# Kernel optimization log

Measured on AMD Instinct MI355X. Metric: run time of the kernel, lower is better.

## Reference

```python
import jax, jax.numpy as jnp
import numpy as np

EPS = 1e-06

def setup_inputs() -> dict:
    key = jax.random.key(0)
    k1, k2, k3, k4, k5 = jax.random.split(key, 5)
    B, T, D, Dv = 4, 2048, 128, 128
    q = jax.random.normal(k1, (B, T, D), dtype=jnp.float32)
    k = jax.random.normal(k2, (B, T, D), dtype=jnp.float32)
    v = jax.random.normal(k3, (B, T, Dv), dtype=jnp.float32)
    # phi = nn.Linear(dim, dim) followed by ELU; torch Linear default init ~ U(-1/sqrt(D), 1/sqrt(D))
    lim = 1.0 / np.sqrt(D)
    W_phi = jax.random.uniform(k4, (D, D), minval=-lim, maxval=lim, dtype=jnp.float32)
    b_phi = jax.random.uniform(k5, (D,), minval=-lim, maxval=lim, dtype=jnp.float32)
    return {"q": q, "k": k, "v": v, "W_phi": W_phi, "b_phi": b_phi}

def reference(q, k, v, W_phi, b_phi):
    # feature map: phi(x) = ELU(x @ W^T + b) + 1  (positive features)
    def phi(x):
        return jax.nn.elu(jnp.einsum('btd,ed->bte', x, W_phi) + b_phi) + 1.0

    Q = phi(q)                      # [B,T,D]
    K = phi(k)                      # [B,T,D]
    # causal recurrent state (zero initial state since h=None):
    # z_t = sum_{tau<=t} K_tau                 -> [B,T,D]
    # s_t = sum_{tau<=t} K_tau (outer) v_tau   -> [B,T,D,Dv]
    z = jnp.cumsum(K, axis=1)
    s = jnp.cumsum(K[..., :, None] * v[..., None, :], axis=1)
    den = jnp.einsum('btd,btd->bt', Q, z) + EPS          # [B,T]
    out = jnp.einsum('btd,btde->bte', Q, s) / den[..., None]  # [B,T,Dv]
    return out
```

## Files before the change

kernel.cpp:

```cpp
#include <hip/hip_runtime.h>
#include <hip/hip_bf16.h>

#define BB 4
#define TT 2048
#define DD 128
#define CHK 64
#define NCHK 32
#define NCHKS (BB*NCHK)

typedef __attribute__((ext_vector_type(8))) short  bf16x8;
typedef __attribute__((ext_vector_type(4))) float  f32x4;

#define MFMA(a,b,c) __builtin_amdgcn_mfma_f32_16x16x32_bf16(a, b, c, 0, 0, 0)

__device__ __forceinline__ short f2b(float f) {
    union { float f; unsigned u; } x; x.f = f;
    unsigned r = x.u + 0x7fffu + ((x.u >> 16) & 1u);
    return (short)(r >> 16);
}
__device__ __forceinline__ float b2f(short s) {
    union { unsigned u; float f; } x; x.u = ((unsigned)(unsigned short)s) << 16;
    return x.f;
}
__device__ __forceinline__ bf16x8 cvt8(const float* p) {
    float4 a = *(const float4*)p, b = *(const float4*)(p + 4);
    bf16x8 r;
    r[0]=f2b(a.x); r[1]=f2b(a.y); r[2]=f2b(a.z); r[3]=f2b(a.w);
    r[4]=f2b(b.x); r[5]=f2b(b.y); r[6]=f2b(b.z); r[7]=f2b(b.w);
    return r;
}

__global__ __launch_bounds__(256, 2) void k1_chunk(const float* __restrict__ q,
                                                   const float* __restrict__ kin,
                                                   const float* __restrict__ vin,
                                                   const float* __restrict__ W,
                                                   const float* __restrict__ bias,
                                                   short* __restrict__ Ss_g,
                                                   float* __restrict__ zc_g,
                                                   short* __restrict__ vT_g,
                                                   short* __restrict__ Qf_g,
                                                   short* __restrict__ Kf_g) {
    int c = blockIdx.x >> 1, dh = blockIdx.x & 1;
    int d0 = 64 * dh;
    const float* qc = q   + (size_t)c * CHK * DD;
    const float* kc = kin + (size_t)c * CHK * DD;
    const float* vc = vin + (size_t)c * CHK * DD;

    __shared__ __align__(16) short Wl [64][DD + 8];
    __shared__ __align__(16) short KfT[64][CHK + 8];
    __shared__ __align__(16) short vT [DD][CHK + 8];
    __shared__ __align__(16) short stage[2][CHK][CHK + 8];

    int tid = threadIdx.x, lane = tid & 63, w = tid >> 6;
    int l15 = lane & 15, l4 = lane >> 4;
    const f32x4 z4 = {0.f, 0.f, 0.f, 0.f};

    bf16x8 afk[4], afq[4];
    {
        int row = 16 * w + l15;
        #pragma unroll
        for (int kk = 0; kk < 4; ++kk) {
            afk[kk] = cvt8(kc + row * DD + kk * 32 + l4 * 8);
            afq[kk] = cvt8(qc + row * DD + kk * 32 + l4 * 8);
        }
    }
    #pragma unroll
    for (int it = 0; it < 8; ++it) {
        int i = tid + it * 256;
        int row = i >> 5, c4 = (i & 31) * 4;
        float4 v = *(const float4*)(W + (size_t)(d0 + row) * DD + c4);
        unsigned lo = (unsigned short)f2b(v.x) | ((unsigned)(unsigned short)f2b(v.y) << 16);
        unsigned hi = (unsigned short)f2b(v.z) | ((unsigned)(unsigned short)f2b(v.w) << 16);
        uint2 p; p.x = lo; p.y = hi;
        *(uint2*)&Wl[row][c4] = p;
    }
    #pragma unroll
    for (int it = 0; it < 8; ++it) {
        int i = tid + it * 256;
        int t = i >> 5, e4 = (i & 31) * 4;
        float4 vv = *(const float4*)(vc + t * DD + e4);
        vT[e4 + 0][t] = f2b(vv.x); vT[e4 + 1][t] = f2b(vv.y);
        vT[e4 + 2][t] = f2b(vv.z); vT[e4 + 3][t] = f2b(vv.w);
    }
    __syncthreads();

    #pragma unroll
    for (int n = 0; n < 4; ++n) {
        int dl = 16 * n + l15;
        f32x4 dk = z4, dq = z4;
        #pragma unroll
        for (int kk = 0; kk < 4; ++kk) {
            bf16x8 bw = *(const bf16x8*)&Wl[dl][kk * 32 + l4 * 8];
            dk = MFMA(afk[kk], bw, dk);
            dq = MFMA(afq[kk], bw, dq);
        }
        float bv = bias[d0 + dl];
        #pragma unroll
        for (int j = 0; j < 4; ++j) {
            int t = 16 * w + l4 * 4 + j;
            float zk = dk[j] + bv;
            short rk = f2b((zk > 0.f) ? (zk + 1.f) : __expf(zk));
            KfT[dl][t] = rk;
            stage[0][t][dl] = rk;
            float zq = dq[j] + bv;
            stage[1][t][dl] = f2b((zq > 0.f) ? (zq + 1.f) : __expf(zq));
        }
    }
    __syncthreads();

    {
        short* dk_ = Kf_g + (size_t)c * CHK * DD + d0;
        short* dq_ = Qf_g + (size_t)c * CHK * DD + d0;
        #pragma unroll
        for (int it = 0; it < 2; ++it) {
            int i = tid + it * 256;
            int t = i >> 3, u = (i & 7) * 8;
            *(bf16x8*)(dk_ + t * DD + u) = *(const bf16x8*)&stage[0][t][u];
            *(bf16x8*)(dq_ + t * DD + u) = *(const bf16x8*)&stage[1][t][u];
        }
    }
    if (tid < 64) {
        float s = 0.f;
        #pragma unroll
        for (int t8 = 0; t8 < CHK / 8; ++t8) {
            bf16x8 kv = *(const bf16x8*)&KfT[tid][t8 * 8];
            #pragma unroll
            for (int j = 0; j < 8; ++j) s += b2f(kv[j]);
        }
        zc_g[(size_t)c * DD + d0 + tid] = s;
    }
    if (dh == 0) {
        #pragma unroll
        for (int it = 0; it < 4; ++it) {
            int i = tid + it * 256;
            int e = i >> 3, t0 = (i & 7) * 8;
            *(bf16x8*)(vT_g + (size_t)c * DD * CHK + e * CHK + t0) =
                *(const bf16x8*)&vT[e][t0];
        }
    }

    f32x4 sacc[8];
    #pragma unroll
    for (int n = 0; n < 8; ++n) sacc[n] = z4;
    #pragma unroll
    for (int kk = 0; kk < 2; ++kk) {
        bf16x8 afr = *(const bf16x8*)&KfT[16 * w + l15][kk * 32 + l4 * 8];
        #pragma unroll
        for (int n = 0; n < 8; ++n) {
            bf16x8 bfr = *(const bf16x8*)&vT[16 * n + l15][kk * 32 + l4 * 8];
            sacc[n] = MFMA(afr, bfr, sacc[n]);
        }
    }
    __syncthreads();

    short (*st)[CHK + 8] = (short(*)[CHK + 8])&stage[0][0][0];
    #pragma unroll
    for (int n = 0; n < 8; ++n) {
        int e = 16 * n + l15;
        #pragma unroll
        for (int j = 0; j < 4; ++j)
            st[e][16 * w + l4 * 4 + j] = f2b(sacc[n][j]);
    }
    __syncthreads();

    short* dst = Ss_g + (size_t)c * DD * DD + d0;
    #pragma unroll
    for (int it = 0; it < 4; ++it) {
        int i = tid + it * 256;
        int e = i >> 3, u = (i & 7) * 8;
        *(bf16x8*)(dst + e * DD + u) = *(const bf16x8*)&st[e][u];
    }
}

__global__ __launch_bounds__(128) void k2_scan(const short* __restrict__ Ss_g,
                                               const float* __restrict__ zc_g,
                                               short* __restrict__ Sp_g,
                                               float* __restrict__ zp_g) {
    int e = blockIdx.x & 127, b = blockIdx.x >> 7;
    int d = threadIdx.x;
    size_t base = ((size_t)(b * NCHK) * DD + e) * DD + d;
    const size_t stride = (size_t)DD * DD;

    float vals[NCHK];
    #pragma unroll
    for (int c2 = 0; c2 < NCHK; ++c2) vals[c2] = b2f(Ss_g[base + c2 * stride]);
    float run = 0.f;
    #pragma unroll
    for (int c2 = 0; c2 < NCHK; ++c2) {
        Sp_g[base + c2 * stride] = f2b(run);
        run += vals[c2];
    }
    if (e == 0) {
        float vz[NCHK];
        #pragma unroll
        for (int c2 = 0; c2 < NCHK; ++c2) vz[c2] = zc_g[(size_t)(b * NCHK + c2) * DD + d];
        float rz = 0.f;
        #pragma unroll
        for (int c2 = 0; c2 < NCHK; ++c2) {
            zp_g[(size_t)(b * NCHK + c2) * DD + d] = rz;
            rz += vz[c2];
        }
    }
}

__global__ __launch_bounds__(256) void k3_out(const short* __restrict__ Qf_g,
                                              const short* __restrict__ Kf_g,
                                              const short* __restrict__ Sp_g,
                                              const float* __restrict__ zp_g,
                                              const short* __restrict__ vT_g,
                                              float* __restrict__ out) {
    int c = blockIdx.x >> 1, h = blockIdx.x & 1;

    __shared__ __align__(16) short Qf[CHK][DD + 8];
    __shared__ __align__(16) short Kf[CHK][DD + 8];
    __shared__ __align__(16) short Ps[CHK][CHK + 8];
    __shared__ float den[CHK];

    int tid = threadIdx.x, lane = tid & 63, w = tid >> 6;
    int l15 = lane & 15, l4 = lane >> 4;
    const f32x4 z4 = {0.f, 0.f, 0.f, 0.f};

    const float* zp = zp_g + (size_t)c * DD;
    bf16x8 bz[4];
    #pragma unroll
    for (int kk = 0; kk < 4; ++kk) {
        bf16x8 zf = cvt8(zp + kk * 32 + l4 * 8);
        bf16x8 zero = {0,0,0,0,0,0,0,0};
        bz[kk] = (l15 == 0) ? zf : zero;
    }

    {
        const short* srcq = Qf_g + (size_t)c * CHK * DD;
        const short* srck = Kf_g + (size_t)c * CHK * DD;
        #pragma unroll
        for (int it = 0; it < 4; ++it) {
            int i = tid + it * 256;
            int t = i >> 4, u = (i & 15) * 8;
            *(bf16x8*)&Qf[t][u] = *(const bf16x8*)(srcq + t * DD + u);
            *(bf16x8*)&Kf[t][u] = *(const bf16x8*)(srck + t * DD + u);
        }
    }
    __syncthreads();

    bf16x8 aq[4];
    #pragma unroll
    for (int kk = 0; kk < 4; ++kk)
        aq[kk] = *(const bf16x8*)&Qf[16 * w + l15][kk * 32 + l4 * 8];

    f32x4 p4 = z4;
    #pragma unroll
    for (int kk = 0; kk < 4; ++kk) p4 = MFMA(aq[kk], bz[kk], p4);

    float rs[4] = {0.f, 0.f, 0.f, 0.f};
    #pragma unroll
    for (int n2 = 0; n2 < 4; ++n2) {
        f32x4 p = z4;
        #pragma unroll
        for (int kk = 0; kk < 4; ++kk) {
            bf16x8 bk = *(const bf16x8*)&Kf[16 * n2 + l15][kk * 32 + l4 * 8];
            p = MFMA(aq[kk], bk, p);
        }
        int t2 = 16 * n2 + l15;
        #pragma unroll
        for (int j = 0; j < 4; ++j) {
            int t = 16 * w + l4 * 4 + j;
            float pm = (t2 <= t) ? p[j] : 0.f;
            Ps[t][t2] = f2b(pm);
            rs[j] += pm;
        }
    }
    #pragma unroll
    for (int off = 1; off < 16; off <<= 1) {
        #pragma unroll
        for (int j = 0; j < 4; ++j) rs[j] += __shfl_xor(rs[j], off);
    }
    if (l15 == 0) {
        #pragma unroll
        for (int j = 0; j < 4; ++j)
            den[16 * w + l4 * 4 + j] = rs[j] + p4[j] + 1e-6f;
    }

    bf16x8 ap[2];
    #pragma unroll
    for (int kk = 0; kk < 2; ++kk)
        ap[kk] = *(const bf16x8*)&Ps[16 * w + l15][kk * 32 + l4 * 8];

    const short* Sp  = Sp_g + (size_t)c * DD * DD;
    const short* vTg = vT_g + (size_t)c * DD * CHK;
    f32x4 oacc[4];
    #pragma unroll
    for (int n = 0; n < 4; ++n) oacc[n] = z4;
    #pragma unroll
    for (int n = 0; n < 4; ++n) {
        int e = 64 * h + 16 * n + l15;
        #pragma unroll
        for (int kk = 0; kk < 4; ++kk) {
            bf16x8 bs = *(const bf16x8*)(Sp + e * DD + kk * 32 + l4 * 8);
            oacc[n] = MFMA(aq[kk], bs, oacc[n]);
        }
        #pragma unroll
        for (int kk = 0; kk < 2; ++kk) {
            bf16x8 bv = *(const bf16x8*)(vTg + e * CHK + kk * 32 + l4 * 8);
            oacc[n] = MFMA(ap[kk], bv, oacc[n]);
        }
    }

    float* oc = out + (size_t)c * CHK * DD;
    float invs[4];
    #pragma unroll
    for (int j = 0; j < 4; ++j) invs[j] = 1.0f / den[16 * w + l4 * 4 + j];
    #pragma unroll
    for (int n = 0; n < 4; ++n) {
        int e = 64 * h + 16 * n + l15;
        #pragma unroll
        for (int j = 0; j < 4; ++j) {
            int t = 16 * w + l4 * 4 + j;
            oc[t * DD + e] = oacc[n][j] * invs[j];
        }
    }
}

extern "C" void kernel_launch(void* const* d_in, const int* in_sizes, int n_in,
                              void* d_out, int out_size, void* d_ws, size_t ws_size,
                              hipStream_t stream) {
    const float* q  = (const float*)d_in[0];
    const float* k  = (const float*)d_in[1];
    const float* v  = (const float*)d_in[2];
    const float* W  = (const float*)d_in[3];
    const float* bi = (const float*)d_in[4];
    float* out = (float*)d_out;

    float* zc_g = (float*)d_ws;
    float* zp_g = zc_g + (size_t)NCHKS * DD;
    short* Ss_g = (short*)(zp_g + (size_t)NCHKS * DD);
    short* Sp_g = Ss_g + (size_t)NCHKS * DD * DD;
    short* vT_g = Sp_g + (size_t)NCHKS * DD * DD;
    short* Qf_g = vT_g + (size_t)NCHKS * DD * CHK;
    short* Kf_g = Qf_g + (size_t)NCHKS * CHK * DD;

    k1_chunk<<<2 * NCHKS, 256, 0, stream>>>(q, k, v, W, bi, Ss_g, zc_g, vT_g, Qf_g, Kf_g);
    k2_scan<<<512, 128, 0, stream>>>(Ss_g, zc_g, Sp_g, zp_g);
    k3_out<<<2 * NCHKS, 256, 0, stream>>>(Qf_g, Kf_g, Sp_g, zp_g, vT_g, out);
}
```

Before: 27.02 us.

## Merge split-D chunk blocks into one 1024-thread block per chunk

The first kernel now runs one 1024-thread block per chunk instead of two 256-thread blocks that each handle half of the feature dimension. This stops duplicating the q/k/v loads and the v transpose across the two half-blocks, and q/k are staged through LDS so all 16 waves share them. In exchange, there are only 128 blocks on the GPU, each with a much larger LDS footprint, which lowers occupancy and parallelism. The block also adds an extra barrier.

```diff
diff --git a/kernel.cpp b/kernel.cpp
--- a/kernel.cpp
+++ b/kernel.cpp
@@ -30,53 +30,51 @@
     return r;
 }
 
-__global__ __launch_bounds__(256, 2) void k1_chunk(const float* __restrict__ q,
-                                                   const float* __restrict__ kin,
-                                                   const float* __restrict__ vin,
-                                                   const float* __restrict__ W,
-                                                   const float* __restrict__ bias,
-                                                   short* __restrict__ Ss_g,
-                                                   float* __restrict__ zc_g,
-                                                   short* __restrict__ vT_g,
-                                                   short* __restrict__ Qf_g,
-                                                   short* __restrict__ Kf_g) {
-    int c = blockIdx.x >> 1, dh = blockIdx.x & 1;
-    int d0 = 64 * dh;
+__global__ __launch_bounds__(1024) void k1_chunk(const float* __restrict__ q,
+                                                 const float* __restrict__ kin,
+                                                 const float* __restrict__ vin,
+                                                 const float* __restrict__ W,
+                                                 const float* __restrict__ bias,
+                                                 short* __restrict__ Ss_g,
+                                                 float* __restrict__ zc_g,
+                                                 short* __restrict__ vT_g,
+                                                 short* __restrict__ Qf_g,
+                                                 short* __restrict__ Kf_g) {
+    int c = blockIdx.x;
     const float* qc = q   + (size_t)c * CHK * DD;
     const float* kc = kin + (size_t)c * CHK * DD;
     const float* vc = vin + (size_t)c * CHK * DD;
 
-    __shared__ __align__(16) short Wl [64][DD + 8];
-    __shared__ __align__(16) short KfT[64][CHK + 8];
+    __shared__ __align__(16) short Wl [DD][DD + 8];
+    __shared__ __align__(16) short qs [CHK][DD + 8];
+    __shared__ __align__(16) short ks [CHK][DD + 8];
+    __shared__ __align__(16) short KfT[DD][CHK + 8];
     __shared__ __align__(16) short vT [DD][CHK + 8];
-    __shared__ __align__(16) short stage[2][CHK][CHK + 8];
+    __shared__ __align__(16) short st [DD][DD + 8];
 
     int tid = threadIdx.x, lane = tid & 63, w = tid >> 6;
     int l15 = lane & 15, l4 = lane >> 4;
+    int tq = w & 3, eh = w >> 2;
     const f32x4 z4 = {0.f, 0.f, 0.f, 0.f};
 
-    bf16x8 afk[4], afq[4];
-    {
-        int row = 16 * w + l15;
-        #pragma unroll
-        for (int kk = 0; kk < 4; ++kk) {
-            afk[kk] = cvt8(kc + row * DD + kk * 32 + l4 * 8);
-            afq[kk] = cvt8(qc + row * DD + kk * 32 + l4 * 8);
-        }
-    }
-    #pragma unroll
-    for (int it = 0; it < 8; ++it) {
-        int i = tid + it * 256;
+    #pragma unroll
+    for (int it = 0; it < 4; ++it) {
+        int i = tid + it * 1024;
         int row = i >> 5, c4 = (i & 31) * 4;
-        float4 v = *(const float4*)(W + (size_t)(d0 + row) * DD + c4);
+        float4 v = *(const float4*)(W + (size_t)row * DD + c4);
         unsigned lo = (unsigned short)f2b(v.x) | ((unsigned)(unsigned short)f2b(v.y) << 16);
         unsigned hi = (unsigned short)f2b(v.z) | ((unsigned)(unsigned short)f2b(v.w) << 16);
         uint2 p; p.x = lo; p.y = hi;
         *(uint2*)&Wl[row][c4] = p;
     }
-    #pragma unroll
-    for (int it = 0; it < 8; ++it) {
-        int i = tid + it * 256;
+    {
+        int row = tid >> 4, col8 = (tid & 15) * 8;
+        *(bf16x8*)&qs[row][col8] = cvt8(qc + row * DD + col8);
+        *(bf16x8*)&ks[row][col8] = cvt8(kc + row * DD + col8);
+    }
+    #pragma unroll
+    for (int it = 0; it < 2; ++it) {
+        int i = tid + it * 1024;
         int t = i >> 5, e4 = (i & 31) * 4;
         float4 vv = *(const float4*)(vc + t * DD + e4);
         vT[e4 + 0][t] = f2b(vv.x); vT[e4 + 1][t] = f2b(vv.y);
@@ -84,42 +82,47 @@
     }
     __syncthreads();
 
-    #pragma unroll
-    for (int n = 0; n < 4; ++n) {
-        int dl = 16 * n + l15;
-        f32x4 dk = z4, dq = z4;
+    bf16x8 afq[4], afk[4];
+    {
+        int row = 16 * tq + l15;
         #pragma unroll
         for (int kk = 0; kk < 4; ++kk) {
-            bf16x8 bw = *(const bf16x8*)&Wl[dl][kk * 32 + l4 * 8];
+            afq[kk] = *(const bf16x8*)&qs[row][kk * 32 + l4 * 8];
+            afk[kk] = *(const bf16x8*)&ks[row][kk * 32 + l4 * 8];
+        }
+    }
+    __syncthreads();
+
+    #pragma unroll
+    for (int n = 0; n < 2; ++n) {
+        int e = 32 * eh + 16 * n + l15;
+        f32x4 dq = z4, dk = z4;
+        #pragma unroll
+        for (int kk = 0; kk < 4; ++kk) {
+            bf16x8 bw = *(const bf16x8*)&Wl[e][kk * 32 + l4 * 8];
+            dq = MFMA(afq[kk], bw, dq);
             dk = MFMA(afk[kk], bw, dk);
-            dq = MFMA(afq[kk], bw, dq);
-        }
-        float bv = bias[d0 + dl];
+        }
+        float bv = bias[e];
         #pragma unroll
         for (int j = 0; j < 4; ++j) {
-            int t = 16 * w + l4 * 4 + j;
+            int t = 16 * tq + l4 * 4 + j;
+            float zq = dq[j] + bv;
+            qs[t][e] = f2b((zq > 0.f) ? (zq + 1.f) : __expf(zq));
             float zk = dk[j] + bv;
             short rk = f2b((zk > 0.f) ? (zk + 1.f) : __expf(zk));
-            KfT[dl][t] = rk;
-            stage[0][t][dl] = rk;
-            float zq = dq[j] + bv;
-            stage[1][t][dl] = f2b((zq > 0.f) ? (zq + 1.f) : __expf(zq));
-        }
-    }
-    __syncthreads();
-
-    {
-        short* dk_ = Kf_g + (size_t)c * CHK * DD + d0;
-        short* dq_ = Qf_g + (size_t)c * CHK * DD + d0;
-        #pragma unroll
-        for (int it = 0; it < 2; ++it) {
-            int i = tid + it * 256;
-            int t = i >> 3, u = (i & 7) * 8;
-            *(bf16x8*)(dk_ + t * DD + u) = *(const bf16x8*)&stage[0][t][u];
-            *(bf16x8*)(dq_ + t * DD + u) = *(const bf16x8*)&stage[1][t][u];
-        }
-    }
-    if (tid < 64) {
+            ks[t][e] = rk;
+            KfT[e][t] = rk;
+        }
+    }
+    __syncthreads();
+
+    {
+        int t = tid >> 4, u = (tid & 15) * 8;
+        *(bf16x8*)(Qf_g + (size_t)c * CHK * DD + t * DD + u) = *(const bf16x8*)&qs[t][u];
+        *(bf16x8*)(Kf_g + (size_t)c * CHK * DD + t * DD + u) = *(const bf16x8*)&ks[t][u];
+    }
+    if (tid < DD) {
         float s = 0.f;
         #pragma unroll
         for (int t8 = 0; t8 < CHK / 8; ++t8) {
@@ -127,47 +130,42 @@
             #pragma unroll
             for (int j = 0; j < 8; ++j) s += b2f(kv[j]);
         }
-        zc_g[(size_t)c * DD + d0 + tid] = s;
-    }
-    if (dh == 0) {
-        #pragma unroll
-        for (int it = 0; it < 4; ++it) {
-            int i = tid + it * 256;
-            int e = i >> 3, t0 = (i & 7) * 8;
-            *(bf16x8*)(vT_g + (size_t)c * DD * CHK + e * CHK + t0) =
-                *(const bf16x8*)&vT[e][t0];
-        }
-    }
-
-    f32x4 sacc[8];
-    #pragma unroll
-    for (int n = 0; n < 8; ++n) sacc[n] = z4;
-    #pragma unroll
-    for (int kk = 0; kk < 2; ++kk) {
-        bf16x8 afr = *(const bf16x8*)&KfT[16 * w + l15][kk * 32 + l4 * 8];
-        #pragma unroll
-        for (int n = 0; n < 8; ++n) {
-            bf16x8 bfr = *(const bf16x8*)&vT[16 * n + l15][kk * 32 + l4 * 8];
-            sacc[n] = MFMA(afr, bfr, sacc[n]);
-        }
-    }
-    __syncthreads();
-
-    short (*st)[CHK + 8] = (short(*)[CHK + 8])&stage[0][0][0];
-    #pragma unroll
-    for (int n = 0; n < 8; ++n) {
-        int e = 16 * n + l15;
-        #pragma unroll
-        for (int j = 0; j < 4; ++j)
-            st[e][16 * w + l4 * 4 + j] = f2b(sacc[n][j]);
-    }
-    __syncthreads();
-
-    short* dst = Ss_g + (size_t)c * DD * DD + d0;
-    #pragma unroll
-    for (int it = 0; it < 4; ++it) {
-        int i = tid + it * 256;
-        int e = i >> 3, u = (i & 7) * 8;
+        zc_g[(size_t)c * DD + tid] = s;
+    }
+    {
+        int e = tid >> 3, t0 = (tid & 7) * 8;
+        *(bf16x8*)(vT_g + (size_t)c * DD * CHK + e * CHK + t0) = *(const bf16x8*)&vT[e][t0];
+    }
+
+    {
+        int dt = w >> 1, nb = 4 * (w & 1);
+        f32x4 sacc[4];
+        #pragma unroll
+        for (int n = 0; n < 4; ++n) sacc[n] = z4;
+        #pragma unroll
+        for (int kk = 0; kk < 2; ++kk) {
+            bf16x8 afr = *(const bf16x8*)&KfT[16 * dt + l15][kk * 32 + l4 * 8];
+            #pragma unroll
+            for (int n = 0; n < 4; ++n) {
+                bf16x8 bfr = *(const bf16x8*)&vT[16 * (nb + n) + l15][kk * 32 + l4 * 8];
+                sacc[n] = MFMA(afr, bfr, sacc[n]);
+            }
+        }
+        #pragma unroll
+        for (int n = 0; n < 4; ++n) {
+            int e = 16 * (nb + n) + l15;
+            #pragma unroll
+            for (int j = 0; j < 4; ++j)
+                st[e][16 * dt + l4 * 4 + j] = f2b(sacc[n][j]);
+        }
+    }
+    __syncthreads();
+
+    short* dst = Ss_g + (size_t)c * DD * DD;
+    #pragma unroll
+    for (int it = 0; it < 2; ++it) {
+        int i = tid + it * 1024;
+        int e = i >> 4, u = (i & 15) * 8;
         *(bf16x8*)(dst + e * DD + u) = *(const bf16x8*)&st[e][u];
     }
 }
@@ -338,7 +336,7 @@
     short* Qf_g = vT_g + (size_t)NCHKS * DD * CHK;
     short* Kf_g = Qf_g + (size_t)NCHKS * CHK * DD;
 
-    k1_chunk<<<2 * NCHKS, 256, 0, stream>>>(q, k, v, W, bi, Ss_g, zc_g, vT_g, Qf_g, Kf_g);
+    k1_chunk<<<NCHKS, 1024, 0, stream>>>(q, k, v, W, bi, Ss_g, zc_g, vT_g, Qf_g, Kf_g);
     k2_scan<<<512, 128, 0, stream>>>(Ss_g, zc_g, Sp_g, zp_g);
     k3_out<<<2 * NCHKS, 256, 0, stream>>>(Qf_g, Kf_g, Sp_g, zp_g, vT_g, out);
 }
```

New measurement: 28.41 us. +5.1%, slower.

## Split chunk kernel by time halves instead of feature halves, sum partial states in scan

Applied to the files above, without the earlier changes.

Each chunk-kernel block now handles 32 timesteps with all 128 features, where before it handled all 64 timesteps for half the features. This avoids recomputing the q/k feature-map projection twice per chunk and the duplicated loads. Each half writes its own partial chunk state and key sum, and the scan kernel adds the two. The cost is a second full bf16 state buffer to write and read, extra rounding of partial sums, and a larger shared-memory footprint for the full W tile.

```diff
diff --git a/kernel.cpp b/kernel.cpp
--- a/kernel.cpp
+++ b/kernel.cpp
@@ -35,145 +35,157 @@
                                                    const float* __restrict__ vin,
                                                    const float* __restrict__ W,
                                                    const float* __restrict__ bias,
-                                                   short* __restrict__ Ss_g,
-                                                   float* __restrict__ zc_g,
+                                                   short* __restrict__ Ssa_g,
+                                                   short* __restrict__ Ssb_g,
+                                                   float* __restrict__ za_g,
+                                                   float* __restrict__ zb_g,
                                                    short* __restrict__ vT_g,
                                                    short* __restrict__ Qf_g,
                                                    short* __restrict__ Kf_g) {
-    int c = blockIdx.x >> 1, dh = blockIdx.x & 1;
-    int d0 = 64 * dh;
-    const float* qc = q   + (size_t)c * CHK * DD;
-    const float* kc = kin + (size_t)c * CHK * DD;
-    const float* vc = vin + (size_t)c * CHK * DD;
-
-    __shared__ __align__(16) short Wl [64][DD + 8];
-    __shared__ __align__(16) short KfT[64][CHK + 8];
-    __shared__ __align__(16) short vT [DD][CHK + 8];
-    __shared__ __align__(16) short stage[2][CHK][CHK + 8];
+    int c = blockIdx.x >> 1, th = blockIdx.x & 1;
+    int t0 = 32 * th;
+    const float* qc = q   + (size_t)(c * CHK + t0) * DD;
+    const float* kc = kin + (size_t)(c * CHK + t0) * DD;
+    const float* vc = vin + (size_t)(c * CHK + t0) * DD;
+
+    __shared__ __align__(16) short Wst[DD][DD + 8];
+    __shared__ __align__(16) short qs [32][DD + 8];
+    __shared__ __align__(16) short ks [32][DD + 8];
+    __shared__ __align__(16) short KfT[DD][32 + 8];
+    __shared__ __align__(16) short vT [DD][32 + 8];
 
     int tid = threadIdx.x, lane = tid & 63, w = tid >> 6;
     int l15 = lane & 15, l4 = lane >> 4;
+    int tq = w & 1, eh = w >> 1;
     const f32x4 z4 = {0.f, 0.f, 0.f, 0.f};
 
-    bf16x8 afk[4], afq[4];
-    {
-        int row = 16 * w + l15;
-        #pragma unroll
-        for (int kk = 0; kk < 4; ++kk) {
-            afk[kk] = cvt8(kc + row * DD + kk * 32 + l4 * 8);
-            afq[kk] = cvt8(qc + row * DD + kk * 32 + l4 * 8);
-        }
-    }
-    #pragma unroll
-    for (int it = 0; it < 8; ++it) {
+    #pragma unroll
+    for (int it = 0; it < 16; ++it) {
         int i = tid + it * 256;
         int row = i >> 5, c4 = (i & 31) * 4;
-        float4 v = *(const float4*)(W + (size_t)(d0 + row) * DD + c4);
+        float4 v = *(const float4*)(W + (size_t)row * DD + c4);
         unsigned lo = (unsigned short)f2b(v.x) | ((unsigned)(unsigned short)f2b(v.y) << 16);
         unsigned hi = (unsigned short)f2b(v.z) | ((unsigned)(unsigned short)f2b(v.w) << 16);
         uint2 p; p.x = lo; p.y = hi;
-        *(uint2*)&Wl[row][c4] = p;
-    }
-    #pragma unroll
-    for (int it = 0; it < 8; ++it) {
-        int i = tid + it * 256;
-        int t = i >> 5, e4 = (i & 31) * 4;
-        float4 vv = *(const float4*)(vc + t * DD + e4);
-        vT[e4 + 0][t] = f2b(vv.x); vT[e4 + 1][t] = f2b(vv.y);
-        vT[e4 + 2][t] = f2b(vv.z); vT[e4 + 3][t] = f2b(vv.w);
+        *(uint2*)&Wst[row][c4] = p;
+    }
+    #pragma unroll
+    for (int it = 0; it < 2; ++it) {
+        int i = tid + it * 256;
+        int tl = i >> 4, col8 = (i & 15) * 8;
+        *(bf16x8*)&qs[tl][col8] = cvt8(qc + tl * DD + col8);
+        *(bf16x8*)&ks[tl][col8] = cvt8(kc + tl * DD + col8);
+    }
+    #pragma unroll
+    for (int it = 0; it < 4; ++it) {
+        int i = tid + it * 256;
+        int tl = i >> 5, e4 = (i & 31) * 4;
+        float4 vv = *(const float4*)(vc + tl * DD + e4);
+        vT[e4 + 0][tl] = f2b(vv.x); vT[e4 + 1][tl] = f2b(vv.y);
+        vT[e4 + 2][tl] = f2b(vv.z); vT[e4 + 3][tl] = f2b(vv.w);
+    }
+    __syncthreads();
+
+    bf16x8 afq[4], afk[4];
+    {
+        int row = 16 * tq + l15;
+        #pragma unroll
+        for (int kk = 0; kk < 4; ++kk) {
+            afq[kk] = *(const bf16x8*)&qs[row][kk * 32 + l4 * 8];
+            afk[kk] = *(const bf16x8*)&ks[row][kk * 32 + l4 * 8];
+        }
     }
     __syncthreads();
 
     #pragma unroll
     for (int n = 0; n < 4; ++n) {
-        int dl = 16 * n + l15;
-        f32x4 dk = z4, dq = z4;
+        int e = 64 * eh + 16 * n + l15;
+        f32x4 dq = z4, dk = z4;
         #pragma unroll
         for (int kk = 0; kk < 4; ++kk) {
-            bf16x8 bw = *(const bf16x8*)&Wl[dl][kk * 32 + l4 * 8];
+            bf16x8 bw = *(const bf16x8*)&Wst[e][kk * 32 + l4 * 8];
+            dq = MFMA(afq[kk], bw, dq);
             dk = MFMA(afk[kk], bw, dk);
-            dq = MFMA(afq[kk], bw, dq);
-        }
-        float bv = bias[d0 + dl];
+        }
+        float bv = bias[e];
         #pragma unroll
         for (int j = 0; j < 4; ++j) {
-            int t = 16 * w + l4 * 4 + j;
+            int tl = 16 * tq + l4 * 4 + j;
+            float zq = dq[j] + bv;
+            qs[tl][e] = f2b((zq > 0.f) ? (zq + 1.f) : __expf(zq));
             float zk = dk[j] + bv;
             short rk = f2b((zk > 0.f) ? (zk + 1.f) : __expf(zk));
-            KfT[dl][t] = rk;
-            stage[0][t][dl] = rk;
-            float zq = dq[j] + bv;
-            stage[1][t][dl] = f2b((zq > 0.f) ? (zq + 1.f) : __expf(zq));
-        }
-    }
-    __syncthreads();
-
-    {
-        short* dk_ = Kf_g + (size_t)c * CHK * DD + d0;
-        short* dq_ = Qf_g + (size_t)c * CHK * DD + d0;
-        #pragma unroll
-        for (int it = 0; it < 2; ++it) {
-            int i = tid + it * 256;
-            int t = i >> 3, u = (i & 7) * 8;
-            *(bf16x8*)(dk_ + t * DD + u) = *(const bf16x8*)&stage[0][t][u];
-            *(bf16x8*)(dq_ + t * DD + u) = *(const bf16x8*)&stage[1][t][u];
-        }
-    }
-    if (tid < 64) {
+            ks[tl][e] = rk;
+            KfT[e][tl] = rk;
+        }
+    }
+    __syncthreads();
+
+    #pragma unroll
+    for (int it = 0; it < 2; ++it) {
+        int i = tid + it * 256;
+        int tl = i >> 4, u = (i & 15) * 8;
+        size_t off = ((size_t)c * CHK + t0 + tl) * DD + u;
+        *(bf16x8*)(Qf_g + off) = *(const bf16x8*)&qs[tl][u];
+        *(bf16x8*)(Kf_g + off) = *(const bf16x8*)&ks[tl][u];
+    }
+    if (tid < DD) {
         float s = 0.f;
         #pragma unroll
-        for (int t8 = 0; t8 < CHK / 8; ++t8) {
+        for (int t8 = 0; t8 < 4; ++t8) {
             bf16x8 kv = *(const bf16x8*)&KfT[tid][t8 * 8];
             #pragma unroll
             for (int j = 0; j < 8; ++j) s += b2f(kv[j]);
         }
-        zc_g[(size_t)c * DD + d0 + tid] = s;
-    }
-    if (dh == 0) {
-        #pragma unroll
-        for (int it = 0; it < 4; ++it) {
-            int i = tid + it * 256;
-            int e = i >> 3, t0 = (i & 7) * 8;
-            *(bf16x8*)(vT_g + (size_t)c * DD * CHK + e * CHK + t0) =
-                *(const bf16x8*)&vT[e][t0];
-        }
-    }
-
-    f32x4 sacc[8];
-    #pragma unroll
-    for (int n = 0; n < 8; ++n) sacc[n] = z4;
-    #pragma unroll
-    for (int kk = 0; kk < 2; ++kk) {
-        bf16x8 afr = *(const bf16x8*)&KfT[16 * w + l15][kk * 32 + l4 * 8];
+        (th ? zb_g : za_g)[(size_t)c * DD + tid] = s;
+    }
+    #pragma unroll
+    for (int it = 0; it < 2; ++it) {
+        int i = tid + it * 256;
+        int e = i >> 2, tb = (i & 3) * 8;
+        *(bf16x8*)(vT_g + (size_t)c * DD * CHK + e * CHK + t0 + tb) =
+            *(const bf16x8*)&vT[e][tb];
+    }
+
+    f32x4 sacc[2][8];
+    {
+        bf16x8 afr[2];
+        #pragma unroll
+        for (int mi = 0; mi < 2; ++mi)
+            afr[mi] = *(const bf16x8*)&KfT[16 * (2 * w + mi) + l15][l4 * 8];
         #pragma unroll
         for (int n = 0; n < 8; ++n) {
-            bf16x8 bfr = *(const bf16x8*)&vT[16 * n + l15][kk * 32 + l4 * 8];
-            sacc[n] = MFMA(afr, bfr, sacc[n]);
-        }
-    }
-    __syncthreads();
-
-    short (*st)[CHK + 8] = (short(*)[CHK + 8])&stage[0][0][0];
-    #pragma unroll
-    for (int n = 0; n < 8; ++n) {
-        int e = 16 * n + l15;
-        #pragma unroll
-        for (int j = 0; j < 4; ++j)
-            st[e][16 * w + l4 * 4 + j] = f2b(sacc[n][j]);
-    }
-    __syncthreads();
-
-    short* dst = Ss_g + (size_t)c * DD * DD + d0;
-    #pragma unroll
-    for (int it = 0; it < 4; ++it) {
-        int i = tid + it * 256;
-        int e = i >> 3, u = (i & 7) * 8;
-        *(bf16x8*)(dst + e * DD + u) = *(const bf16x8*)&st[e][u];
-    }
-}
-
-__global__ __launch_bounds__(128) void k2_scan(const short* __restrict__ Ss_g,
-                                               const float* __restrict__ zc_g,
+            bf16x8 bfr = *(const bf16x8*)&vT[16 * n + l15][l4 * 8];
+            sacc[0][n] = MFMA(afr[0], bfr, z4);
+            sacc[1][n] = MFMA(afr[1], bfr, z4);
+        }
+    }
+    __syncthreads();
+
+    #pragma unroll
+    for (int mi = 0; mi < 2; ++mi)
+        #pragma unroll
+        for (int n = 0; n < 8; ++n) {
+            int e = 16 * n + l15;
+            #pragma unroll
+            for (int j = 0; j < 4; ++j)
+                Wst[e][16 * (2 * w + mi) + l4 * 4 + j] = f2b(sacc[mi][n][j]);
+        }
+    __syncthreads();
+
+    short* dst = (th ? Ssb_g : Ssa_g) + (size_t)c * DD * DD;
+    #pragma unroll
+    for (int it = 0; it < 8; ++it) {
+        int i = tid + it * 256;
+        int e = i >> 4, u = (i & 15) * 8;
+        *(bf16x8*)(dst + e * DD + u) = *(const bf16x8*)&Wst[e][u];
+    }
+}
+
+__global__ __launch_bounds__(128) void k2_scan(const short* __restrict__ Ssa_g,
+                                               const short* __restrict__ Ssb_g,
+                                               const float* __restrict__ za_g,
+                                               const float* __restrict__ zb_g,
                                                short* __restrict__ Sp_g,
                                                float* __restrict__ zp_g) {
     int e = blockIdx.x & 127, b = blockIdx.x >> 7;
@@ -183,7 +195,8 @@
 
     float vals[NCHK];
     #pragma unroll
-    for (int c2 = 0; c2 < NCHK; ++c2) vals[c2] = b2f(Ss_g[base + c2 * stride]);
+    for (int c2 = 0; c2 < NCHK; ++c2)
+        vals[c2] = b2f(Ssa_g[base + c2 * stride]) + b2f(Ssb_g[base + c2 * stride]);
     float run = 0.f;
     #pragma unroll
     for (int c2 = 0; c2 < NCHK; ++c2) {
@@ -193,7 +206,10 @@
     if (e == 0) {
         float vz[NCHK];
         #pragma unroll
-        for (int c2 = 0; c2 < NCHK; ++c2) vz[c2] = zc_g[(size_t)(b * NCHK + c2) * DD + d];
+        for (int c2 = 0; c2 < NCHK; ++c2) {
+            size_t iz = (size_t)(b * NCHK + c2) * DD + d;
+            vz[c2] = za_g[iz] + zb_g[iz];
+        }
         float rz = 0.f;
         #pragma unroll
         for (int c2 = 0; c2 < NCHK; ++c2) {
@@ -330,15 +346,18 @@
     const float* bi = (const float*)d_in[4];
     float* out = (float*)d_out;
 
-    float* zc_g = (float*)d_ws;
-    float* zp_g = zc_g + (size_t)NCHKS * DD;
-    short* Ss_g = (short*)(zp_g + (size_t)NCHKS * DD);
-    short* Sp_g = Ss_g + (size_t)NCHKS * DD * DD;
-    short* vT_g = Sp_g + (size_t)NCHKS * DD * DD;
-    short* Qf_g = vT_g + (size_t)NCHKS * DD * CHK;
-    short* Kf_g = Qf_g + (size_t)NCHKS * CHK * DD;
-
-    k1_chunk<<<2 * NCHKS, 256, 0, stream>>>(q, k, v, W, bi, Ss_g, zc_g, vT_g, Qf_g, Kf_g);
-    k2_scan<<<512, 128, 0, stream>>>(Ss_g, zc_g, Sp_g, zp_g);
+    float* za_g = (float*)d_ws;
+    float* zb_g = za_g + (size_t)NCHKS * DD;
+    float* zp_g = zb_g + (size_t)NCHKS * DD;
+    short* Ssa_g = (short*)(zp_g + (size_t)NCHKS * DD);
+    short* Ssb_g = Ssa_g + (size_t)NCHKS * DD * DD;
+    short* Sp_g  = Ssb_g + (size_t)NCHKS * DD * DD;
+    short* vT_g  = Sp_g + (size_t)NCHKS * DD * DD;
+    short* Qf_g  = vT_g + (size_t)NCHKS * DD * CHK;
+    short* Kf_g  = Qf_g + (size_t)NCHKS * CHK * DD;
+
+    k1_chunk<<<2 * NCHKS, 256, 0, stream>>>(q, k, v, W, bi, Ssa_g, Ssb_g,
+                                            za_g, zb_g, vT_g, Qf_g, Kf_g);
+    k2_scan<<<512, 128, 0, stream>>>(Ssa_g, Ssb_g, za_g, zb_g, Sp_g, zp_g);
     k3_out<<<2 * NCHKS, 256, 0, stream>>>(Qf_g, Kf_g, Sp_g, zp_g, vT_g, out);
 }
```

Result: slower. 29.12 us (+7.7%).
